# Kernel optimization log

Measured on AMD Instinct MI355X. Metric: run time of the kernel, lower is better.

The kernel has to match this reference:

```python
import jax, jax.numpy as jnp
import numpy as np

D_MODEL = 1024
NUM_HEADS = 16


def setup_inputs() -> dict:
    key = jax.random.key(0)
    ks = jax.random.split(key, 11)
    B, S, D = 2, 2048, D_MODEL
    s = 1.0 / np.sqrt(D)
    return {
        "queries": jax.random.normal(ks[0], (B, S, D), jnp.float32),
        "keys": jax.random.normal(ks[1], (B, S, D), jnp.float32),
        "values": jax.random.normal(ks[2], (B, S, D), jnp.float32),
        "W_q": jax.random.normal(ks[3], (D, D), jnp.float32) * s,
        "b_q": jnp.zeros((D,), jnp.float32),
        "W_k": jax.random.normal(ks[4], (D, D), jnp.float32) * s,
        "b_k": jnp.zeros((D,), jnp.float32),
        "W_v": jax.random.normal(ks[5], (D, D), jnp.float32) * s,
        "b_v": jnp.zeros((D,), jnp.float32),
        "W_o": jax.random.normal(ks[6], (D, D), jnp.float32) * s,
        "b_o": jnp.zeros((D,), jnp.float32),
    }


def _split_heads(x, num_heads):
    # [B, S, D] -> [B, H, S, d_h]
    B, S, D = x.shape
    return x.reshape(B, S, num_heads, D // num_heads).transpose(0, 2, 1, 3)


def reference(queries, keys, values, W_q, b_q, W_k, b_k, W_v, b_v, W_o, b_o):
    H = NUM_HEADS
    Q = _split_heads(queries @ W_q.T + b_q, H)  # [B,H,S,dh]
    K = _split_heads(keys @ W_k.T + b_k, H)
    V = _split_heads(values @ W_v.T + b_v, H)
    d = Q.shape[-1]
    scores = jnp.einsum("bhqd,bhkd->bhqk", Q, K) / jnp.sqrt(jnp.asarray(d, Q.dtype))
    attn = jax.nn.softmax(scores, axis=-1)
    out = jnp.einsum("bhqk,bhkd->bhqd", attn, V)  # [B,H,S,dh]
    B, _, S, _ = out.shape
    out = out.transpose(0, 2, 1, 3).reshape(B, S, -1)  # combine heads
    return out @ W_o.T + b_o
```

## Files before the change

### kernel.cpp

```cpp
#include <hip/hip_runtime.h>
#include <cstdint>
#include <cmath>

typedef short s16x8 __attribute__((ext_vector_type(8)));
typedef short s16x4 __attribute__((ext_vector_type(4)));
typedef float f32x4 __attribute__((ext_vector_type(4)));
typedef unsigned int u32;

#define AS_G __attribute__((address_space(1)))
#define AS_L __attribute__((address_space(3)))

#define QSCALE 0.18033688011112042f

__device__ __forceinline__ void ld16_to_lds(const void* g, const void* l) {
    __builtin_amdgcn_global_load_lds((AS_G void*)(g), (AS_L void*)(l), 16, 0, 0);
}

__device__ __forceinline__ short f2bf(float f) {
    union { float f; uint32_t u; } v; v.f = f;
    uint32_t r = v.u + 0x7fffu + ((v.u >> 16) & 1u);
    return (short)(r >> 16);
}
__device__ __forceinline__ short f2bf_fast(float f) {
    union { float f; uint32_t u; } v; v.f = f;
    return (short)((v.u + 0x8000u) >> 16);
}

template<int F32OUT, int NJ, int QKV>
__global__ __launch_bounds__(256, 3)
void gemm_bt(const short* __restrict__ Abase, long Az,
             const short* __restrict__ Wbase, long Wz,
             const float* __restrict__ bias0, const float* __restrict__ bias1,
             const float* __restrict__ bias2,
             void* __restrict__ Obase, long Oz,
             const int M, const int N, const int K)
{
    constexpr int BN = NJ * 32;
    constexpr int BSt = (BN * 4) / 256;
    constexpr int LPS = 2 + BSt;
    __shared__ __align__(16) short As[3][128 * 32];
    __shared__ __align__(16) short Bs[3][BN * 32];

    const int t = threadIdx.x, lane = t & 63, wv = t >> 6;
    const int wr = wv >> 1, wc = wv & 1;
    const int q4 = lane >> 4, l16 = lane & 15;

    const u32 gx = gridDim.x, gy = gridDim.y;
    u32 lin = blockIdx.x + gx * (blockIdx.y + gy * blockIdx.z);
    const u32 nwg = gx * gy * gridDim.z;
    if ((nwg & 7u) == 0u) lin = (lin & 7u) * (nwg >> 3) + (lin >> 3);
    const int bxs = lin % gx;
    const u32 rem = lin / gx;
    const int bys = rem % gy;
    const int z   = rem / gy;

    const short* A  = Abase + (long)z * Az;
    const short* Bt = Wbase + (long)z * Wz;
    const float* bias = (z == 0) ? bias0 : ((z == 1) ? bias1 : bias2);
    const float bmul = (QKV && z == 0) ? QSCALE : 1.0f;
    const int bn0 = bxs * BN, bm0 = bys * 128;

    f32x4 acc[4][NJ] = {};

    const short* gA[2];
    const short* gB[BSt];
    #pragma unroll
    for (int s = 0; s < 2; ++s) {
        const int c = t + 256 * s;
        const int r = c >> 2, g = (c & 3) ^ ((c >> 3) & 3);
        gA[s] = A + (size_t)(bm0 + r) * K + g * 8;
    }
    #pragma unroll
    for (int s = 0; s < BSt; ++s) {
        const int c = t + 256 * s;
        const int r = c >> 2, g = (c & 3) ^ ((c >> 3) & 3);
        gB[s] = Bt + (size_t)(bn0 + r) * K + g * 8;
    }

    auto stage = [&](int buf) {
        #pragma unroll
        for (int s = 0; s < 2; ++s) {
            ld16_to_lds(gA[s], &As[buf][(wv * 64 + 256 * s) * 8]);
            gA[s] += 32;
        }
        #pragma unroll
        for (int s = 0; s < BSt; ++s) {
            ld16_to_lds(gB[s], &Bs[buf][(wv * 64 + 256 * s) * 8]);
            gB[s] += 32;
        }
    };

    const int kIters = K >> 5;
    stage(0);
    stage(1);
    for (int kt = 0; kt < kIters; ++kt) {
        const int cur = kt % 3;
        if (kt < kIters - 1)
            asm volatile("s_waitcnt vmcnt(%0)" :: "n"(LPS) : "memory");
        else
            asm volatile("s_waitcnt vmcnt(0)" ::: "memory");
        __builtin_amdgcn_s_barrier();
        __builtin_amdgcn_sched_barrier(0);
        if (kt + 2 < kIters) stage((kt + 2) % 3);

        s16x8 aF[4], bF[NJ];
        #pragma unroll
        for (int i = 0; i < 4; ++i) {
            const int m = wr * 64 + i * 16 + l16;
            aF[i] = *(const s16x8*)&As[cur][m * 32 + (q4 ^ ((m >> 1) & 3)) * 8];
        }
        #pragma unroll
        for (int j = 0; j < NJ; ++j) {
            const int n = wc * (BN / 2) + j * 16 + l16;
            bF[j] = *(const s16x8*)&Bs[cur][n * 32 + (q4 ^ ((n >> 1) & 3)) * 8];
        }
        #pragma unroll
        for (int i = 0; i < 4; ++i)
            #pragma unroll
            for (int j = 0; j < NJ; ++j)
                acc[i][j] = __builtin_amdgcn_mfma_f32_16x16x32_bf16(
                    aF[i], bF[j], acc[i][j], 0, 0, 0);
    }

    #pragma unroll
    for (int j = 0; j < NJ; ++j) {
        const int col = bn0 + wc * (BN / 2) + j * 16 + l16;
        const float bj = bias[col] * bmul;
        #pragma unroll
        for (int i = 0; i < 4; ++i) {
            const int row0 = bm0 + wr * 64 + i * 16 + q4 * 4;
            if (QKV && z == 2) {
                s16x4 ov;
                #pragma unroll
                for (int r = 0; r < 4; ++r) ov[r] = f2bf(acc[i][j][r] + bj);
                *(s16x4*)(((short*)Obase + (long)z * Oz) +
                          (size_t)col * 4096 + row0) = ov;
            } else {
                #pragma unroll
                for (int r = 0; r < 4; ++r) {
                    const float v = acc[i][j][r] + bj;
                    if (F32OUT)
                        ((float*)Obase + (long)z * Oz)[(size_t)(row0 + r) * N + col] = v;
                    else
                        ((short*)Obase + (long)z * Oz)[(size_t)(row0 + r) * N + col] = f2bf(v);
                }
            }
        }
    }
}

__global__ __launch_bounds__(256, 4)
void attn_fwd(const short* __restrict__ Qp, const short* __restrict__ Kp,
              const short* __restrict__ VpT, short* __restrict__ Out)
{
    constexpr int D = 1024, S = 2048;
    __shared__ __align__(16) short Ks[2][512 * 8];
    __shared__ __align__(16) short Vt[2][512 * 8];
    __shared__ __align__(16) short Ps[4 * 16 * 64];

    const int t = threadIdx.x, lane = t & 63, wv = t >> 6;
    const int q4 = lane >> 4, l16 = lane & 15;
    const int bid = blockIdx.x;
    const int qt = (bid >> 3) & 31;
    const int hb = (bid & 7) * 4 + (bid >> 8);
    const int h = hb >> 1, b = hb & 1;
    const size_t rowB = (size_t)b * S;
    const int cb = h * 64;
    const int qrow0 = qt * 64 + wv * 16;
    short* PsW = &Ps[wv * (16 * 64)];

    s16x8 qF[2];
    #pragma unroll
    for (int tk = 0; tk < 2; ++tk)
        qF[tk] = *(const s16x8*)
            &Qp[(rowB + qrow0 + l16) * D + cb + tk * 32 + q4 * 8];

    f32x4 oacc[4] = {};
    f32x4 lacc = {};
    s16x8 onesF;
    #pragma unroll
    for (int e = 0; e < 8; ++e) onesF[e] = (short)0x3F80;

    const short* KpB = Kp + rowB * D + cb;
    const short* VtG = VpT + (size_t)cb * 4096 + b * 2048;

    auto stageKV = [&](int buf, int kv0) {
        #pragma unroll
        for (int s = 0; s < 2; ++s) {
            const int slot = (4 * s + wv) * 64 + lane;
            const int r = slot >> 3;
            const int kcs = (slot & 7) ^ ((r >> 2) & 7);
            ld16_to_lds(KpB + (size_t)(kv0 + r) * D + kcs * 8,
                        &Ks[buf][(wv * 64 + 256 * s) * 8]);
        }
        #pragma unroll
        for (int s = 0; s < 2; ++s) {
            const int c = t + 256 * s;
            const int d = c >> 3, kcp = c & 7;
            ld16_to_lds(VtG + (size_t)d * 4096 + kv0 + ((kcp ^ (d & 7)) * 8),
                        &Vt[buf][(wv * 64 + 256 * s) * 8]);
        }
    };

    stageKV(0, 0);

    for (int kvt = 0; kvt < 32; ++kvt) {
        const int kv0 = kvt * 64;
        __syncthreads();
        if (kvt < 31) stageKV((kvt + 1) & 1, kv0 + 64);

        f32x4 acc[4] = {};
        #pragma unroll
        for (int tk = 0; tk < 2; ++tk) {
            s16x8 kF[4];
            #pragma unroll
            for (int j = 0; j < 4; ++j)
                kF[j] = *(const s16x8*)
                    &Ks[kvt & 1][((4 * l16 + j) * 8 +
                                  ((tk * 4 + q4) ^ (l16 & 7))) * 8];
            #pragma unroll
            for (int j = 0; j < 4; ++j)
                acc[j] = __builtin_amdgcn_mfma_f32_16x16x32_bf16(
                    qF[tk], kF[j], acc[j], 0, 0, 0);
        }

        #pragma unroll
        for (int r = 0; r < 4; ++r) {
            const int m = q4 * 4 + r;
            s16x4 pv;
            #pragma unroll
            for (int j = 0; j < 4; ++j)
                pv[j] = f2bf_fast(__builtin_amdgcn_exp2f(acc[j][r]));
            *(s16x4*)((char*)PsW + m * 128 + ((l16 * 8) ^ ((m & 7) << 4))) = pv;
        }

        #pragma unroll
        for (int tk = 0; tk < 2; ++tk) {
            const s16x8 pF = *(const s16x8*)
                ((const char*)PsW + l16 * 128 +
                 ((tk * 64 + q4 * 16) ^ ((l16 & 7) << 4)));
            lacc = __builtin_amdgcn_mfma_f32_16x16x32_bf16(
                pF, onesF, lacc, 0, 0, 0);
            #pragma unroll
            for (int jd = 0; jd < 4; ++jd) {
                const int d = jd * 16 + l16;
                const s16x8 vF = *(const s16x8*)
                    &Vt[kvt & 1][(d * 8 + ((tk * 4 + q4) ^ (d & 7))) * 8];
                oacc[jd] = __builtin_amdgcn_mfma_f32_16x16x32_bf16(
                    pF, vF, oacc[jd], 0, 0, 0);
            }
        }
    }

    #pragma unroll
    for (int r = 0; r < 4; ++r) {
        const float inv = 1.0f / lacc[r];
        const size_t row = rowB + qrow0 + q4 * 4 + r;
        #pragma unroll
        for (int jd = 0; jd < 4; ++jd)
            Out[row * D + cb + jd * 16 + l16] = f2bf(oacc[jd][r] * inv);
    }
}

__global__ __launch_bounds__(256)
void cast_all(const float* __restrict__ q, const float* __restrict__ k,
              const float* __restrict__ v, const float* __restrict__ wq,
              const float* __restrict__ wk, const float* __restrict__ wv,
              const float* __restrict__ wo, short* __restrict__ out)
{
    const size_t i = ((size_t)blockIdx.x * 256 + threadIdx.x) * 8;
    const float* src; size_t off;
    if      (i < 4194304)  { src = q;  off = i; }
    else if (i < 8388608)  { src = k;  off = i - 4194304; }
    else if (i < 12582912) { src = v;  off = i - 8388608; }
    else if (i < 13631488) { src = wq; off = i - 12582912; }
    else if (i < 14680064) { src = wk; off = i - 13631488; }
    else if (i < 15728640) { src = wv; off = i - 14680064; }
    else                   { src = wo; off = i - 15728640; }
    const float m = (i >= 12582912 && i < 13631488) ? QSCALE : 1.0f;
    const float4 a = *(const float4*)(src + off);
    const float4 c = *(const float4*)(src + off + 4);
    s16x8 o;
    o[0] = f2bf(a.x * m); o[1] = f2bf(a.y * m); o[2] = f2bf(a.z * m); o[3] = f2bf(a.w * m);
    o[4] = f2bf(c.x * m); o[5] = f2bf(c.y * m); o[6] = f2bf(c.z * m); o[7] = f2bf(c.w * m);
    *(s16x8*)(out + i) = o;
}

extern "C" void kernel_launch(void* const* d_in, const int* in_sizes, int n_in,
                              void* d_out, int out_size, void* d_ws, size_t ws_size,
                              hipStream_t stream)
{
    const float* q  = (const float*)d_in[0];
    const float* k  = (const float*)d_in[1];
    const float* v  = (const float*)d_in[2];
    const float* Wq = (const float*)d_in[3];
    const float* bq = (const float*)d_in[4];
    const float* Wk = (const float*)d_in[5];
    const float* bk = (const float*)d_in[6];
    const float* Wv = (const float*)d_in[7];
    const float* bv = (const float*)d_in[8];
    const float* Wo = (const float*)d_in[9];
    const float* bo = (const float*)d_in[10];

    short* ws = (short*)d_ws;
    const long MEL = 1048576;
    short* Aq  = ws;
    short* Wqb = ws + 12 * MEL;
    short* Wob = ws + 15 * MEL;
    short* Qp  = ws + 16 * MEL;
    short* Kp  = ws + 20 * MEL;
    short* VpT = ws + 24 * MEL;
    short* AO  = ws;

    cast_all<<<8192, 256, 0, stream>>>(q, k, v, Wq, Wk, Wv, Wo, ws);

    gemm_bt<0, 4, 1><<<dim3(8, 32, 3), 256, 0, stream>>>(
        Aq, 4 * MEL, Wqb, 1 * MEL, bq, bk, bv, Qp, 4 * MEL, 4096, 1024, 1024);

    attn_fwd<<<1024, 256, 0, stream>>>(Qp, Kp, VpT, AO);

    gemm_bt<1, 2, 0><<<dim3(16, 32, 1), 256, 0, stream>>>(
        AO, 0, Wob, 0, bo, bo, bo, d_out, 0, 4096, 1024, 1024);
}
```

Before: 223.2 us.

## Keep softmax probabilities in registers via permlane swaps instead of LDS round-trip

The attention kernel now computes S^T by swapping MFMA operands (K as A, Q as B). Each lane packs exp2 results with v_cvt_pk_bf16_f32 and rearranges them with v_permlane32/16_swap into the A-operand layout for the PV MFMA, so the per-wave P staging buffer in shared memory is gone. The K LDS swizzle and row mapping change to match the new fragment layout. This removes LDS writes and reads plus the shared-memory footprint per iteration, at the cost of extra cross-lane permute instructions and a different bf16 rounding path.

```diff
diff --git a/kernel.cpp b/kernel.cpp
--- a/kernel.cpp
+++ b/kernel.cpp
@@ -20,10 +20,6 @@
     union { float f; uint32_t u; } v; v.f = f;
     uint32_t r = v.u + 0x7fffu + ((v.u >> 16) & 1u);
     return (short)(r >> 16);
-}
-__device__ __forceinline__ short f2bf_fast(float f) {
-    union { float f; uint32_t u; } v; v.f = f;
-    return (short)((v.u + 0x8000u) >> 16);
 }
 
 template<int F32OUT, int NJ, int QKV>
@@ -156,7 +152,6 @@
     constexpr int D = 1024, S = 2048;
     __shared__ __align__(16) short Ks[2][512 * 8];
     __shared__ __align__(16) short Vt[2][512 * 8];
-    __shared__ __align__(16) short Ps[4 * 16 * 64];
 
     const int t = threadIdx.x, lane = t & 63, wv = t >> 6;
     const int q4 = lane >> 4, l16 = lane & 15;
@@ -167,7 +162,6 @@
     const size_t rowB = (size_t)b * S;
     const int cb = h * 64;
     const int qrow0 = qt * 64 + wv * 16;
-    short* PsW = &Ps[wv * (16 * 64)];
 
     s16x8 qF[2];
     #pragma unroll
@@ -189,7 +183,7 @@
         for (int s = 0; s < 2; ++s) {
             const int slot = (4 * s + wv) * 64 + lane;
             const int r = slot >> 3;
-            const int kcs = (slot & 7) ^ ((r >> 2) & 7);
+            const int kcs = (slot & 7) ^ (r & 7);
             ld16_to_lds(KpB + (size_t)(kv0 + r) * D + kcs * 8,
                         &Ks[buf][(wv * 64 + 256 * s) * 8]);
         }
@@ -212,42 +206,53 @@
         f32x4 acc[4] = {};
         #pragma unroll
         for (int tk = 0; tk < 2; ++tk) {
-            s16x8 kF[4];
+            s16x8 kA[4];
             #pragma unroll
             for (int j = 0; j < 4; ++j)
-                kF[j] = *(const s16x8*)
-                    &Ks[kvt & 1][((4 * l16 + j) * 8 +
+                kA[j] = *(const s16x8*)
+                    &Ks[kvt & 1][((j * 16 + l16) * 8 +
                                   ((tk * 4 + q4) ^ (l16 & 7))) * 8];
             #pragma unroll
             for (int j = 0; j < 4; ++j)
                 acc[j] = __builtin_amdgcn_mfma_f32_16x16x32_bf16(
-                    qF[tk], kF[j], acc[j], 0, 0, 0);
-        }
-
-        #pragma unroll
-        for (int r = 0; r < 4; ++r) {
-            const int m = q4 * 4 + r;
-            s16x4 pv;
-            #pragma unroll
-            for (int j = 0; j < 4; ++j)
-                pv[j] = f2bf_fast(__builtin_amdgcn_exp2f(acc[j][r]));
-            *(s16x4*)((char*)PsW + m * 128 + ((l16 * 8) ^ ((m & 7) << 4))) = pv;
-        }
-
-        #pragma unroll
-        for (int tk = 0; tk < 2; ++tk) {
-            const s16x8 pF = *(const s16x8*)
-                ((const char*)PsW + l16 * 128 +
-                 ((tk * 64 + q4 * 16) ^ ((l16 & 7) << 4)));
+                    kA[j], qF[tk], acc[j], 0, 0, 0);
+        }
+
+        u32 c[4][2];
+        #pragma unroll
+        for (int j = 0; j < 4; ++j) {
+            const float p0 = __builtin_amdgcn_exp2f(acc[j][0]);
+            const float p1 = __builtin_amdgcn_exp2f(acc[j][1]);
+            const float p2 = __builtin_amdgcn_exp2f(acc[j][2]);
+            const float p3 = __builtin_amdgcn_exp2f(acc[j][3]);
+            asm("v_cvt_pk_bf16_f32 %0, %1, %2" : "=v"(c[j][0]) : "v"(p0), "v"(p1));
+            asm("v_cvt_pk_bf16_f32 %0, %1, %2" : "=v"(c[j][1]) : "v"(p2), "v"(p3));
+        }
+
+        union { s16x8 v; u32 w[4]; } pA[2];
+        #pragma unroll
+        for (int tkp = 0; tkp < 2; ++tkp) {
+            #pragma unroll
+            for (int bb = 0; bb < 2; ++bb) {
+                u32 x = c[2 * tkp][bb], y = c[2 * tkp + 1][bb];
+                asm("v_permlane32_swap_b32 %0, %1" : "+v"(x), "+v"(y));
+                asm("v_permlane16_swap_b32 %0, %1" : "+v"(x), "+v"(y));
+                pA[tkp].w[bb] = x;
+                pA[tkp].w[2 + bb] = y;
+            }
+        }
+
+        #pragma unroll
+        for (int tkp = 0; tkp < 2; ++tkp) {
             lacc = __builtin_amdgcn_mfma_f32_16x16x32_bf16(
-                pF, onesF, lacc, 0, 0, 0);
+                pA[tkp].v, onesF, lacc, 0, 0, 0);
             #pragma unroll
             for (int jd = 0; jd < 4; ++jd) {
                 const int d = jd * 16 + l16;
                 const s16x8 vF = *(const s16x8*)
-                    &Vt[kvt & 1][(d * 8 + ((tk * 4 + q4) ^ (d & 7))) * 8];
+                    &Vt[kvt & 1][(d * 8 + ((tkp * 4 + q4) ^ (d & 7))) * 8];
                 oacc[jd] = __builtin_amdgcn_mfma_f32_16x16x32_bf16(
-                    pF, vF, oacc[jd], 0, 0, 0);
+                    pA[tkp].v, vF, oacc[jd], 0, 0, 0);
             }
         }
     }
```

New measurement: 218.0 us. -2.3%, faster.
